# Kernel tuning notes

Hardware: AMD Instinct MI355X
Metric: run time of the kernel (lower is better)

## Reference

```python
import jax, jax.numpy as jnp
import numpy as np

HEADS = 16
DIM_HEAD = 64
DIM = 1024
EPS = 1e-5


def _layernorm(x, g, b):
    mu = jnp.mean(x, axis=-1, keepdims=True)
    var = jnp.var(x, axis=-1, keepdims=True)
    return (x - mu) * jax.lax.rsqrt(var + EPS) * g + b


def setup_inputs() -> dict:
    key = jax.random.key(0)
    ks = jax.random.split(key, 8)
    inner = HEADS * DIM_HEAD  # 1024
    x = jax.random.normal(ks[0], (2, 2048, DIM), dtype=jnp.float32)
    w_qkv = jax.random.normal(ks[1], (DIM, inner * 3), dtype=jnp.float32) * (DIM ** -0.5)
    w_out = jax.random.normal(ks[2], (inner, DIM), dtype=jnp.float32) * (inner ** -0.5)
    ln1_g = jnp.ones((DIM,), jnp.float32)
    ln1_b = jnp.zeros((DIM,), jnp.float32)
    ln2_g = jnp.ones((DIM,), jnp.float32)
    ln2_b = jnp.zeros((DIM,), jnp.float32)
    return {"x": x, "ln1_g": ln1_g, "ln1_b": ln1_b, "w_qkv": w_qkv,
            "w_out": w_out, "ln2_g": ln2_g, "ln2_b": ln2_b}


def reference(x, ln1_g, ln1_b, w_qkv, w_out, ln2_g, ln2_b):
    b, n, _ = x.shape
    scale = DIM_HEAD ** -0.5
    xn = _layernorm(x, ln1_g, ln1_b)
    qkv = xn @ w_qkv  # [b, n, 3*inner]
    q, k, v = jnp.split(qkv, 3, axis=-1)
    # b n (h d) -> b h n d
    resh = lambda t: t.reshape(b, n, HEADS, DIM_HEAD).transpose(0, 2, 1, 3)
    q, k, v = resh(q) * scale, resh(k), resh(v)
    sim = jnp.einsum('bhid,bhjd->bhij', q, k)
    causal = jnp.tril(jnp.ones((n, n), dtype=bool))
    # masked_fill(triu(1), 0) followed by relu == relu masked to lower triangle
    attn = jnp.where(causal, jax.nn.relu(sim), 0.0)
    out = jnp.einsum('bhij,bhjd->bhid', attn, v)
    out = out.transpose(0, 2, 1, 3).reshape(b, n, HEADS * DIM_HEAD)
    return _layernorm(out @ w_out, ln2_g, ln2_b)
```

## Files before the change

kernel.cpp:

```cpp
#include <hip/hip_runtime.h>
#include <cstdint>
#include <cstddef>


typedef __bf16 bf16_t;
typedef __bf16 bf16x8 __attribute__((ext_vector_type(8)));
typedef __bf16 bf16x4 __attribute__((ext_vector_type(4)));
typedef float  f32x4  __attribute__((ext_vector_type(4)));

#define DEV_INLINE __device__ __forceinline__

DEV_INLINE void async_copy16(void* lds, const void* g) {
  __builtin_amdgcn_global_load_lds(
      (__attribute__((address_space(1))) void*)(g),
      (__attribute__((address_space(3))) void*)(lds), 16, 0, 0);
}

__global__ __launch_bounds__(256) void prep_kernel(
    const float* __restrict__ x, const float* __restrict__ g1,
    const float* __restrict__ b1, bf16_t* __restrict__ xn,
    const float* __restrict__ w_qkv, bf16_t* __restrict__ wqkvT,
    const float* __restrict__ w_out, bf16_t* __restrict__ woutT) {
  const int bid = blockIdx.x;
  const int t = threadIdx.x;
  if (bid < 4096) {
    const int w = t >> 6, l = t & 63;
    const float* xr = x + (size_t)bid * 1024;
    float4 v = *(const float4*)(xr + t * 4);
    float s  = v.x + v.y + v.z + v.w;
    float s2 = v.x * v.x + v.y * v.y + v.z * v.z + v.w * v.w;
    #pragma unroll
    for (int off = 32; off >= 1; off >>= 1) {
      s  += __shfl_down(s, off);
      s2 += __shfl_down(s2, off);
    }
    __shared__ float red[8];
    if (l == 0) { red[w] = s; red[4 + w] = s2; }
    __syncthreads();
    s  = red[0] + red[1] + red[2] + red[3];
    s2 = red[4] + red[5] + red[6] + red[7];
    float mu  = s * (1.0f / 1024.0f);
    float var = s2 * (1.0f / 1024.0f) - mu * mu;
    float rs  = rsqrtf(var + 1e-5f);
    float4 gv = *(const float4*)(g1 + t * 4);
    float4 bv = *(const float4*)(b1 + t * 4);
    bf16x4 o;
    o[0] = (bf16_t)((v.x - mu) * rs * gv.x + bv.x);
    o[1] = (bf16_t)((v.y - mu) * rs * gv.y + bv.y);
    o[2] = (bf16_t)((v.z - mu) * rs * gv.z + bv.z);
    o[3] = (bf16_t)((v.w - mu) * rs * gv.w + bv.w);
    *(bf16x4*)(xn + (size_t)bid * 1024 + t * 4) = o;
  } else {
    const float* wsrc; bf16_t* wdst; int N, tile;
    if (bid < 4864) { wsrc = w_qkv; wdst = wqkvT; N = 3072; tile = bid - 4096; }
    else            { wsrc = w_out; wdst = woutT; N = 1024; tile = bid - 4864; }
    const int ntiles = N >> 6;
    const int n0 = (tile % ntiles) * 64, k0 = (tile / ntiles) * 64;
    __shared__ __align__(16) float tl[64][68];
    #pragma unroll
    for (int c = 0; c < 4; ++c) {
      int idx = c * 256 + t;
      int r = idx >> 4, c4 = (idx & 15) * 4;
      *(float4*)&tl[r][c4] = *(const float4*)(wsrc + (size_t)(k0 + r) * N + n0 + c4);
    }
    __syncthreads();
    #pragma unroll
    for (int c = 0; c < 2; ++c) {
      int idx = c * 256 + t;
      int nl = idx >> 3, kc = (idx & 7) * 8;
      bf16x8 o;
      #pragma unroll
      for (int ii = 0; ii < 8; ++ii) o[ii] = (bf16_t)tl[kc + ii][nl];
      *(bf16x8*)(wdst + (size_t)(n0 + nl) * 1024 + k0 + kc) = o;
    }
  }
}

__global__ __launch_bounds__(256) void ln2_kernel(
    const bf16_t* __restrict__ z0, const bf16_t* __restrict__ z1,
    const float* __restrict__ g, const float* __restrict__ bta,
    float* __restrict__ out) {
  const int row = blockIdx.x;
  const int t = threadIdx.x, w = t >> 6, l = t & 63;
  bf16x4 a0 = *(const bf16x4*)(z0 + (size_t)row * 1024 + t * 4);
  bf16x4 a1 = *(const bf16x4*)(z1 + (size_t)row * 1024 + t * 4);
  float4 v;
  v.x = (float)a0[0] + (float)a1[0];
  v.y = (float)a0[1] + (float)a1[1];
  v.z = (float)a0[2] + (float)a1[2];
  v.w = (float)a0[3] + (float)a1[3];
  float s  = v.x + v.y + v.z + v.w;
  float s2 = v.x * v.x + v.y * v.y + v.z * v.z + v.w * v.w;
  #pragma unroll
  for (int off = 32; off >= 1; off >>= 1) {
    s  += __shfl_down(s, off);
    s2 += __shfl_down(s2, off);
  }
  __shared__ float red[8];
  if (l == 0) { red[w] = s; red[4 + w] = s2; }
  __syncthreads();
  s  = red[0] + red[1] + red[2] + red[3];
  s2 = red[4] + red[5] + red[6] + red[7];
  float mu  = s * (1.0f / 1024.0f);
  float var = s2 * (1.0f / 1024.0f) - mu * mu;
  float rs  = rsqrtf(var + 1e-5f);
  float4 gv = *(const float4*)(g + t * 4);
  float4 bv = *(const float4*)(bta + t * 4);
  float4 o;
  o.x = (v.x - mu) * rs * gv.x + bv.x;
  o.y = (v.y - mu) * rs * gv.y + bv.y;
  o.z = (v.z - mu) * rs * gv.z + bv.z;
  o.w = (v.w - mu) * rs * gv.w + bv.w;
  *(float4*)(out + (size_t)row * 1024 + t * 4) = o;
}

template <int EPI, int KSPLIT>
__global__ __launch_bounds__(256, 3) void gemm128_kernel(
    const bf16_t* __restrict__ A, const bf16_t* __restrict__ Bt,
    void* __restrict__ C0, void* __restrict__ C1, void* __restrict__ C2) {
  __shared__ __align__(16) bf16_t As[128 * 64];
  __shared__ __align__(16) bf16_t Bs[128 * 64];
  const int t = threadIdx.x;
  const int w = t >> 6, l = t & 63, l15 = l & 15, quad = l >> 4;
  const int wy = w >> 1, wx = w & 1;
  const int m0 = blockIdx.y * 128, n0 = blockIdx.x * 128;
  const int kz = (KSPLIT > 1) ? blockIdx.z : 0;
  const int kt0 = kz * (16 / KSPLIT), kt1 = kt0 + (16 / KSPLIT);

  const int r_l = l >> 3;
  const int u_src = (l & 7) ^ r_l;
  const int rswz = l15 & 7;

  f32x4 acc[4][4];
  #pragma unroll
  for (int i = 0; i < 4; ++i)
    #pragma unroll
    for (int j = 0; j < 4; ++j) acc[i][j] = (f32x4)0.0f;

  for (int kt = kt0; kt < kt1; ++kt) {
    __syncthreads();
    #pragma unroll
    for (int c = 0; c < 4; ++c) {
      int idx = w * 4 + c;
      int row = idx * 8 + r_l;
      async_copy16(&As[idx * 512], A + (size_t)(m0 + row) * 1024 + kt * 64 + u_src * 8);
      async_copy16(&Bs[idx * 512], Bt + (size_t)(n0 + row) * 1024 + kt * 64 + u_src * 8);
    }
    __syncthreads();
    #pragma unroll
    for (int kk = 0; kk < 2; ++kk) {
      bf16x8 af[4], bfr[4];
      #pragma unroll
      for (int i = 0; i < 4; ++i)
        af[i] = *(const bf16x8*)&As[(wy * 64 + i * 16 + l15) * 64 + (((kk * 4 + quad) ^ rswz) * 8)];
      #pragma unroll
      for (int j = 0; j < 4; ++j)
        bfr[j] = *(const bf16x8*)&Bs[(wx * 64 + j * 16 + l15) * 64 + (((kk * 4 + quad) ^ rswz) * 8)];
      #pragma unroll
      for (int i = 0; i < 4; ++i)
        #pragma unroll
        for (int j = 0; j < 4; ++j)
          acc[i][j] = __builtin_amdgcn_mfma_f32_16x16x32_bf16(af[i], bfr[j], acc[i][j], 0, 0, 0);
    }
  }

  if (EPI == 0) {
    bf16_t* C = (bf16_t*)(kz == 0 ? C0 : C1);
    #pragma unroll
    for (int i = 0; i < 4; ++i)
      #pragma unroll
      for (int j = 0; j < 4; ++j)
        #pragma unroll
        for (int r = 0; r < 4; ++r) {
          int m = m0 + wy * 64 + i * 16 + quad * 4 + r;
          int n = n0 + wx * 64 + j * 16 + l15;
          C[(size_t)m * 1024 + n] = (bf16_t)acc[i][j][r];
        }
  } else {
    int nb = n0 + wx * 64;
    int which = nb >> 10;
    int head = (nb & 1023) >> 6;
    const int bq = m0 >> 11;
    const int mb = (m0 & 2047) + wy * 64;
    if (which == 2) {
      bf16_t* dst = (bf16_t*)C2 + ((size_t)(bq * 16 + head)) * 64 * 2048;
      #pragma unroll
      for (int i = 0; i < 4; ++i)
        #pragma unroll
        for (int j = 0; j < 4; ++j) {
          bf16x4 pk;
          #pragma unroll
          for (int r = 0; r < 4; ++r) pk[r] = (bf16_t)acc[i][j][r];
          int d = j * 16 + l15;
          int pos = mb + i * 16 + quad * 4;
          *(bf16x4*)(dst + (size_t)d * 2048 + pos) = pk;
        }
    } else {
      bf16_t* dst = which == 0 ? (bf16_t*)C0 : (bf16_t*)C1;
      float sc = which == 0 ? 0.125f : 1.0f;
      #pragma unroll
      for (int i = 0; i < 4; ++i)
        #pragma unroll
        for (int j = 0; j < 4; ++j)
          #pragma unroll
          for (int r = 0; r < 4; ++r) {
            int pos = mb + i * 16 + quad * 4 + r;
            int d = j * 16 + l15;
            dst[(((size_t)(bq * 16 + head)) * 2048 + pos) * 64 + d] =
                (bf16_t)(acc[i][j][r] * sc);
          }
    }
  }
}

__global__ __launch_bounds__(256, 2) void attn_kernel(
    const bf16_t* __restrict__ q, const bf16_t* __restrict__ k,
    const bf16_t* __restrict__ vT, bf16_t* __restrict__ out) {
  __shared__ __align__(16) bf16_t Ks[2][64 * 64];
  __shared__ __align__(16) bf16_t Vts[2][64 * 64];
  __shared__ __align__(16) bf16_t Ss[64 * 72];

  const int h = blockIdx.x, b = blockIdx.z;
  const int j = (b == 0) ? blockIdx.y : 15 - blockIdx.y;
  const int t = threadIdx.x;
  const int w = t >> 6, l = t & 63, l15 = l & 15, quad = l >> 4;
  const size_t bh = (size_t)(b * 16 + h);
  const int rA = 2 * j, rB = 2 * j + 1;
  const int nt = 2 * j + 2;

  const int r_l = l >> 3;
  const int u_g = (l & 7) ^ r_l;
  const int rswz = l15 & 7;

  auto stage_tile = [&](int buf, int kt) {
    #pragma unroll
    for (int c = 0; c < 2; ++c) {
      int idx = w * 2 + c;
      int row = idx * 8 + r_l;
      async_copy16(&Ks[buf][idx * 512],
                   k + (bh * 2048 + kt * 64 + row) * 64 + u_g * 8);
      async_copy16(&Vts[buf][idx * 512],
                   vT + (bh * 64 + row) * 2048 + kt * 64 + u_g * 8);
    }
  };

  auto load_lds = [&](const bf16_t* Kb, const bf16_t* Vb,
                      bf16x8 (&bk)[2][4], bf16x8 (&bv)[2][4]) {
    #pragma unroll
    for (int kk = 0; kk < 2; ++kk)
      #pragma unroll
      for (int tj = 0; tj < 4; ++tj) {
        int u = ((kk * 4 + quad) ^ rswz) * 8;
        bk[kk][tj] = *(const bf16x8*)&Kb[(tj * 16 + l15) * 64 + u];
        bv[kk][tj] = *(const bf16x8*)&Vb[(tj * 16 + l15) * 64 + u];
      }
  };

  bf16x8 qa[2][2];
  {
    #pragma unroll
    for (int kk = 0; kk < 2; ++kk) {
      qa[0][kk] = *(const bf16x8*)(q + (bh * 2048 + rA * 64 + w * 16 + l15) * 64 + kk * 32 + quad * 8);
      qa[1][kk] = *(const bf16x8*)(q + (bh * 2048 + rB * 64 + w * 16 + l15) * 64 + kk * 32 + quad * 8);
    }
  }

  f32x4 acc0[4], acc1[4];
  #pragma unroll
  for (int tj = 0; tj < 4; ++tj) { acc0[tj] = (f32x4)0.0f; acc1[tj] = (f32x4)0.0f; }

  auto sU = [&](f32x4 (&sacc)[4], bf16x8 (&qf)[2], bf16x8 (&bk)[2][4]) {
    #pragma unroll
    for (int tj = 0; tj < 4; ++tj) sacc[tj] = (f32x4)0.0f;
    #pragma unroll
    for (int kk = 0; kk < 2; ++kk)
      #pragma unroll
      for (int tj = 0; tj < 4; ++tj)
        sacc[tj] = __builtin_amdgcn_mfma_f32_16x16x32_bf16(bk[kk][tj], qf[kk], sacc[tj], 0, 0, 0);
  };
  auto wU = [&](f32x4 (&sacc)[4], bool dg) {
    #pragma unroll
    for (int tj = 0; tj < 4; ++tj) {
      bf16x4 pk;
      #pragma unroll
      for (int r = 0; r < 4; ++r) {
        float v = fmaxf(sacc[tj][r], 0.0f);
        if (dg && (tj * 16 + quad * 4 + r > w * 16 + l15)) v = 0.0f;
        pk[r] = (bf16_t)v;
      }
      *(bf16x4*)&Ss[(w * 16 + l15) * 72 + tj * 16 + quad * 4] = pk;
    }
  };
  auto pU = [&](f32x4 (&accr)[4], bf16x8 (&bv)[2][4]) {
    #pragma unroll
    for (int kk = 0; kk < 2; ++kk) {
      bf16x8 as_ = *(const bf16x8*)&Ss[(w * 16 + l15) * 72 + kk * 32 + quad * 8];
      #pragma unroll
      for (int tj = 0; tj < 4; ++tj)
        accr[tj] = __builtin_amdgcn_mfma_f32_16x16x32_bf16(bv[kk][tj], as_, accr[tj], 0, 0, 0);
    }
  };

  stage_tile(0, 0);
  for (int it = 0; it < nt; ++it) {
    __syncthreads();
    if (it + 1 < nt) stage_tile((it + 1) & 1, it + 1);
    const int buf = it & 1;
    bf16x8 bk[2][4], bv[2][4];
    load_lds(Ks[buf], Vts[buf], bk, bv);
    if (it < rB) {
      f32x4 s0[4], s1[4];
      sU(s0, qa[0], bk);
      sU(s1, qa[1], bk);
      wU(s0, it == rA); pU(acc0, bv);
      wU(s1, false);    pU(acc1, bv);
    } else {
      f32x4 s1[4];
      sU(s1, qa[1], bk);
      wU(s1, true); pU(acc1, bv);
    }
  }

  #pragma unroll
  for (int tj = 0; tj < 4; ++tj) {
    bf16x4 p0, p1;
    #pragma unroll
    for (int r = 0; r < 4; ++r) { p0[r] = (bf16_t)acc0[tj][r]; p1[r] = (bf16_t)acc1[tj][r]; }
    int posA = rA * 64 + w * 16 + l15;
    int posB = rB * 64 + w * 16 + l15;
    int col = h * 64 + tj * 16 + quad * 4;
    *(bf16x4*)(out + ((size_t)b * 2048 + posA) * 1024 + col) = p0;
    *(bf16x4*)(out + ((size_t)b * 2048 + posB) * 1024 + col) = p1;
  }
}

extern "C" void kernel_launch(void* const* d_in, const int* in_sizes, int n_in,
                              void* d_out, int out_size, void* d_ws, size_t ws_size,
                              hipStream_t stream) {
  (void)in_sizes; (void)n_in; (void)out_size; (void)ws_size;
  const float* x     = (const float*)d_in[0];
  const float* ln1_g = (const float*)d_in[1];
  const float* ln1_b = (const float*)d_in[2];
  const float* w_qkv = (const float*)d_in[3];
  const float* w_out = (const float*)d_in[4];
  const float* ln2_g = (const float*)d_in[5];
  const float* ln2_b = (const float*)d_in[6];
  float* out = (float*)d_out;

  char* ws = (char*)d_ws;
  bf16_t* xn     = (bf16_t*)(ws + 0);
  bf16_t* wqkvT  = (bf16_t*)(ws + 8388608);
  bf16_t* woutT  = (bf16_t*)(ws + 14680064);
  bf16_t* qb     = (bf16_t*)(ws + 16777216);
  bf16_t* kb     = (bf16_t*)(ws + 25165824);
  bf16_t* vTb    = (bf16_t*)(ws + 41943040);
  bf16_t* ao     = (bf16_t*)(ws + 50331648);
  bf16_t* zb0    = (bf16_t*)(ws + 58720256);
  bf16_t* zb1    = (bf16_t*)(ws + 67108864);

  prep_kernel<<<5120, 256, 0, stream>>>(x, ln1_g, ln1_b, xn, w_qkv, wqkvT, w_out, woutT);
  gemm128_kernel<1, 1><<<dim3(24, 32), 256, 0, stream>>>(xn, wqkvT, qb, kb, vTb);
  attn_kernel<<<dim3(16, 16, 2), 256, 0, stream>>>(qb, kb, vTb, ao);
  gemm128_kernel<0, 2><<<dim3(8, 32, 2), 256, 0, stream>>>(ao, woutT, zb0, zb1, nullptr);
  ln2_kernel<<<4096, 256, 0, stream>>>(zb0, zb1, ln2_g, ln2_b, out);
}
```

Before: 184.6 us.

## Pair short and long causal query rows in 512-thread attention blocks sharing K/V tiles

Each attention block now has 8 waves covering two query-row pairs, j and 15-j, which balances causal work per block. K/V tiles are staged two at a time and shared by both halves, so the long half reuses the tiles the short half also needs. The grid is halved and blocks get twice the threads and LDS. Possible costs are lower occupancy from the larger LDS footprint and idle waves in the short half once its rows are finished.

```diff
diff --git a/kernel.cpp b/kernel.cpp
--- a/kernel.cpp
+++ b/kernel.cpp
@@ -213,34 +213,43 @@
   }
 }
 
-__global__ __launch_bounds__(256, 2) void attn_kernel(
+__global__ __launch_bounds__(512, 2) void attn_kernel(
     const bf16_t* __restrict__ q, const bf16_t* __restrict__ k,
     const bf16_t* __restrict__ vT, bf16_t* __restrict__ out) {
-  __shared__ __align__(16) bf16_t Ks[2][64 * 64];
-  __shared__ __align__(16) bf16_t Vts[2][64 * 64];
-  __shared__ __align__(16) bf16_t Ss[64 * 72];
-
-  const int h = blockIdx.x, b = blockIdx.z;
-  const int j = (b == 0) ? blockIdx.y : 15 - blockIdx.y;
+  __shared__ __align__(16) bf16_t Ks[2][2][64 * 64];
+  __shared__ __align__(16) bf16_t Vts[2][2][64 * 64];
+  __shared__ __align__(16) bf16_t Ss[2][64 * 72];
+
+  const int h = blockIdx.x, j = blockIdx.y, b = blockIdx.z;
   const int t = threadIdx.x;
   const int w = t >> 6, l = t & 63, l15 = l & 15, quad = l >> 4;
+  const int pairSel = w >> 2;
+  const int wl = w & 3;
   const size_t bh = (size_t)(b * 16 + h);
-  const int rA = 2 * j, rB = 2 * j + 1;
-  const int nt = 2 * j + 2;
+  const int r0 = pairSel ? 30 - 2 * j : 2 * j;
+  const int r1 = r0 + 1;
+  const int niter = 16 - j;
 
   const int r_l = l >> 3;
   const int u_g = (l & 7) ^ r_l;
   const int rswz = l15 & 7;
 
-  auto stage_tile = [&](int buf, int kt) {
-    #pragma unroll
-    for (int c = 0; c < 2; ++c) {
-      int idx = w * 2 + c;
+  auto stage_pair = [&](int buf, int i2) {
+    #pragma unroll
+    for (int c = 0; c < 4; ++c) {
+      int op = w * 4 + c;
+      int tau = op >> 4;
+      int rem = op & 15;
+      int mK = rem >> 3;
+      int idx = rem & 7;
+      int kt = 2 * i2 + tau;
       int row = idx * 8 + r_l;
-      async_copy16(&Ks[buf][idx * 512],
-                   k + (bh * 2048 + kt * 64 + row) * 64 + u_g * 8);
-      async_copy16(&Vts[buf][idx * 512],
-                   vT + (bh * 64 + row) * 2048 + kt * 64 + u_g * 8);
+      if (mK == 0)
+        async_copy16(&Ks[buf][tau][idx * 512],
+                     k + (bh * 2048 + kt * 64 + row) * 64 + u_g * 8);
+      else
+        async_copy16(&Vts[buf][tau][idx * 512],
+                     vT + (bh * 64 + row) * 2048 + kt * 64 + u_g * 8);
     }
   };
 
@@ -260,8 +269,8 @@
   {
     #pragma unroll
     for (int kk = 0; kk < 2; ++kk) {
-      qa[0][kk] = *(const bf16x8*)(q + (bh * 2048 + rA * 64 + w * 16 + l15) * 64 + kk * 32 + quad * 8);
-      qa[1][kk] = *(const bf16x8*)(q + (bh * 2048 + rB * 64 + w * 16 + l15) * 64 + kk * 32 + quad * 8);
+      qa[0][kk] = *(const bf16x8*)(q + (bh * 2048 + r0 * 64 + wl * 16 + l15) * 64 + kk * 32 + quad * 8);
+      qa[1][kk] = *(const bf16x8*)(q + (bh * 2048 + r1 * 64 + wl * 16 + l15) * 64 + kk * 32 + quad * 8);
     }
   }
 
@@ -285,39 +294,44 @@
       #pragma unroll
       for (int r = 0; r < 4; ++r) {
         float v = fmaxf(sacc[tj][r], 0.0f);
-        if (dg && (tj * 16 + quad * 4 + r > w * 16 + l15)) v = 0.0f;
+        if (dg && (tj * 16 + quad * 4 + r > wl * 16 + l15)) v = 0.0f;
         pk[r] = (bf16_t)v;
       }
-      *(bf16x4*)&Ss[(w * 16 + l15) * 72 + tj * 16 + quad * 4] = pk;
+      *(bf16x4*)&Ss[pairSel][(wl * 16 + l15) * 72 + tj * 16 + quad * 4] = pk;
     }
   };
   auto pU = [&](f32x4 (&accr)[4], bf16x8 (&bv)[2][4]) {
     #pragma unroll
     for (int kk = 0; kk < 2; ++kk) {
-      bf16x8 as_ = *(const bf16x8*)&Ss[(w * 16 + l15) * 72 + kk * 32 + quad * 8];
+      bf16x8 as_ = *(const bf16x8*)&Ss[pairSel][(wl * 16 + l15) * 72 + kk * 32 + quad * 8];
       #pragma unroll
       for (int tj = 0; tj < 4; ++tj)
         accr[tj] = __builtin_amdgcn_mfma_f32_16x16x32_bf16(bv[kk][tj], as_, accr[tj], 0, 0, 0);
     }
   };
 
-  stage_tile(0, 0);
-  for (int it = 0; it < nt; ++it) {
-    __syncthreads();
-    if (it + 1 < nt) stage_tile((it + 1) & 1, it + 1);
-    const int buf = it & 1;
-    bf16x8 bk[2][4], bv[2][4];
-    load_lds(Ks[buf], Vts[buf], bk, bv);
-    if (it < rB) {
-      f32x4 s0[4], s1[4];
-      sU(s0, qa[0], bk);
-      sU(s1, qa[1], bk);
-      wU(s0, it == rA); pU(acc0, bv);
-      wU(s1, false);    pU(acc1, bv);
-    } else {
-      f32x4 s1[4];
-      sU(s1, qa[1], bk);
-      wU(s1, true); pU(acc1, bv);
+  stage_pair(0, 0);
+  for (int i = 0; i < niter; ++i) {
+    __syncthreads();
+    if (i + 1 < niter) stage_pair((i + 1) & 1, i + 1);
+    const int buf = i & 1;
+    #pragma unroll
+    for (int tau = 0; tau < 2; ++tau) {
+      const int kt = 2 * i + tau;
+      if (kt > r1) continue;
+      bf16x8 bk[2][4], bv[2][4];
+      load_lds(Ks[buf][tau], Vts[buf][tau], bk, bv);
+      if (kt < r1) {
+        f32x4 s0[4], s1[4];
+        sU(s0, qa[0], bk);
+        sU(s1, qa[1], bk);
+        wU(s0, kt == r0); pU(acc0, bv);
+        wU(s1, false);    pU(acc1, bv);
+      } else {
+        f32x4 s1[4];
+        sU(s1, qa[1], bk);
+        wU(s1, true); pU(acc1, bv);
+      }
     }
   }
 
@@ -326,8 +340,8 @@
     bf16x4 p0, p1;
     #pragma unroll
     for (int r = 0; r < 4; ++r) { p0[r] = (bf16_t)acc0[tj][r]; p1[r] = (bf16_t)acc1[tj][r]; }
-    int posA = rA * 64 + w * 16 + l15;
-    int posB = rB * 64 + w * 16 + l15;
+    int posA = r0 * 64 + wl * 16 + l15;
+    int posB = r1 * 64 + wl * 16 + l15;
     int col = h * 64 + tj * 16 + quad * 4;
     *(bf16x4*)(out + ((size_t)b * 2048 + posA) * 1024 + col) = p0;
     *(bf16x4*)(out + ((size_t)b * 2048 + posB) * 1024 + col) = p1;
@@ -360,7 +374,7 @@
 
   prep_kernel<<<5120, 256, 0, stream>>>(x, ln1_g, ln1_b, xn, w_qkv, wqkvT, w_out, woutT);
   gemm128_kernel<1, 1><<<dim3(24, 32), 256, 0, stream>>>(xn, wqkvT, qb, kb, vTb);
-  attn_kernel<<<dim3(16, 16, 2), 256, 0, stream>>>(qb, kb, vTb, ao);
+  attn_kernel<<<dim3(16, 8, 2), 512, 0, stream>>>(qb, kb, vTb, ao);
   gemm128_kernel<0, 2><<<dim3(8, 32, 2), 256, 0, stream>>>(ao, woutT, zb0, zb1, nullptr);
   ln2_kernel<<<4096, 256, 0, stream>>>(zb0, zb1, ln2_g, ln2_b, out);
 }
```

Result: faster. 171.4 us (-7.2%).

## Pair short and long causal query tiles per block to balance attention work

Applied to the files above, without the earlier changes.

Each attention block now handles query tiles m and 31-m instead of two adjacent tiles 2j and 2j+1. This evens out the causal-mask work across blocks, so the heaviest block no longer processes nearly twice the tiles of an average block. The score scratch buffer is split per wave and per query tile, so both score tiles are written before either PV product is computed. The K/V staging loop is reorganised so each wave issues only K or only V copies. The longest block still streams all 32 KV tiles, so the benefit depends on compute rather than load latency dominating.

```diff
diff --git a/kernel.cpp b/kernel.cpp
--- a/kernel.cpp
+++ b/kernel.cpp
@@ -218,15 +218,15 @@
     const bf16_t* __restrict__ vT, bf16_t* __restrict__ out) {
   __shared__ __align__(16) bf16_t Ks[2][64 * 64];
   __shared__ __align__(16) bf16_t Vts[2][64 * 64];
-  __shared__ __align__(16) bf16_t Ss[64 * 72];
-
-  const int h = blockIdx.x, b = blockIdx.z;
-  const int j = (b == 0) ? blockIdx.y : 15 - blockIdx.y;
+  __shared__ __align__(16) bf16_t Ss[4][2][16 * 72];
+
+  const int x = blockIdx.x, h = blockIdx.y, b = blockIdx.z;
+  const int m = ((x & 1) == 0) ? (x >> 1) : 15 - (x >> 1);
   const int t = threadIdx.x;
   const int w = t >> 6, l = t & 63, l15 = l & 15, quad = l >> 4;
   const size_t bh = (size_t)(b * 16 + h);
-  const int rA = 2 * j, rB = 2 * j + 1;
-  const int nt = 2 * j + 2;
+  const int r_lo = m, r_hi = 31 - m;
+  const int niter = 32 - m;
 
   const int r_l = l >> 3;
   const int u_g = (l & 7) ^ r_l;
@@ -234,13 +234,17 @@
 
   auto stage_tile = [&](int buf, int kt) {
     #pragma unroll
-    for (int c = 0; c < 2; ++c) {
-      int idx = w * 2 + c;
+    for (int c = 0; c < 4; ++c) {
+      int op = w * 4 + c;
+      int mK = op >> 3;
+      int idx = op & 7;
       int row = idx * 8 + r_l;
-      async_copy16(&Ks[buf][idx * 512],
-                   k + (bh * 2048 + kt * 64 + row) * 64 + u_g * 8);
-      async_copy16(&Vts[buf][idx * 512],
-                   vT + (bh * 64 + row) * 2048 + kt * 64 + u_g * 8);
+      if (mK == 0)
+        async_copy16(&Ks[buf][idx * 512],
+                     k + (bh * 2048 + kt * 64 + row) * 64 + u_g * 8);
+      else
+        async_copy16(&Vts[buf][idx * 512],
+                     vT + (bh * 64 + row) * 2048 + kt * 64 + u_g * 8);
     }
   };
 
@@ -260,8 +264,8 @@
   {
     #pragma unroll
     for (int kk = 0; kk < 2; ++kk) {
-      qa[0][kk] = *(const bf16x8*)(q + (bh * 2048 + rA * 64 + w * 16 + l15) * 64 + kk * 32 + quad * 8);
-      qa[1][kk] = *(const bf16x8*)(q + (bh * 2048 + rB * 64 + w * 16 + l15) * 64 + kk * 32 + quad * 8);
+      qa[0][kk] = *(const bf16x8*)(q + (bh * 2048 + r_lo * 64 + w * 16 + l15) * 64 + kk * 32 + quad * 8);
+      qa[1][kk] = *(const bf16x8*)(q + (bh * 2048 + r_hi * 64 + w * 16 + l15) * 64 + kk * 32 + quad * 8);
     }
   }
 
@@ -278,7 +282,7 @@
       for (int tj = 0; tj < 4; ++tj)
         sacc[tj] = __builtin_amdgcn_mfma_f32_16x16x32_bf16(bk[kk][tj], qf[kk], sacc[tj], 0, 0, 0);
   };
-  auto wU = [&](f32x4 (&sacc)[4], bool dg) {
+  auto wU = [&](f32x4 (&sacc)[4], bool dg, bf16_t* SsBuf) {
     #pragma unroll
     for (int tj = 0; tj < 4; ++tj) {
       bf16x4 pk;
@@ -288,36 +292,42 @@
         if (dg && (tj * 16 + quad * 4 + r > w * 16 + l15)) v = 0.0f;
         pk[r] = (bf16_t)v;
       }
-      *(bf16x4*)&Ss[(w * 16 + l15) * 72 + tj * 16 + quad * 4] = pk;
-    }
-  };
-  auto pU = [&](f32x4 (&accr)[4], bf16x8 (&bv)[2][4]) {
+      *(bf16x4*)&SsBuf[l15 * 72 + tj * 16 + quad * 4] = pk;
+    }
+  };
+  auto pU = [&](f32x4 (&accr)[4], bf16x8 (&bv)[2][4], const bf16_t* SsBuf) {
     #pragma unroll
     for (int kk = 0; kk < 2; ++kk) {
-      bf16x8 as_ = *(const bf16x8*)&Ss[(w * 16 + l15) * 72 + kk * 32 + quad * 8];
+      bf16x8 as_ = *(const bf16x8*)&SsBuf[l15 * 72 + kk * 32 + quad * 8];
       #pragma unroll
       for (int tj = 0; tj < 4; ++tj)
         accr[tj] = __builtin_amdgcn_mfma_f32_16x16x32_bf16(bv[kk][tj], as_, accr[tj], 0, 0, 0);
     }
   };
 
+  bf16_t* SsA = &Ss[w][0][0];
+  bf16_t* SsB = &Ss[w][1][0];
+
   stage_tile(0, 0);
-  for (int it = 0; it < nt; ++it) {
-    __syncthreads();
-    if (it + 1 < nt) stage_tile((it + 1) & 1, it + 1);
-    const int buf = it & 1;
+  for (int kt = 0; kt < niter; ++kt) {
+    __syncthreads();
+    if (kt + 1 < niter) stage_tile((kt + 1) & 1, kt + 1);
+    const int buf = kt & 1;
     bf16x8 bk[2][4], bv[2][4];
     load_lds(Ks[buf], Vts[buf], bk, bv);
-    if (it < rB) {
+    if (kt <= r_lo) {
       f32x4 s0[4], s1[4];
       sU(s0, qa[0], bk);
       sU(s1, qa[1], bk);
-      wU(s0, it == rA); pU(acc0, bv);
-      wU(s1, false);    pU(acc1, bv);
+      wU(s0, kt == r_lo, SsA);
+      wU(s1, kt == r_hi, SsB);
+      pU(acc0, bv, SsA);
+      pU(acc1, bv, SsB);
     } else {
       f32x4 s1[4];
       sU(s1, qa[1], bk);
-      wU(s1, true); pU(acc1, bv);
+      wU(s1, kt == r_hi, SsB);
+      pU(acc1, bv, SsB);
     }
   }
 
@@ -326,8 +336,8 @@
     bf16x4 p0, p1;
     #pragma unroll
     for (int r = 0; r < 4; ++r) { p0[r] = (bf16_t)acc0[tj][r]; p1[r] = (bf16_t)acc1[tj][r]; }
-    int posA = rA * 64 + w * 16 + l15;
-    int posB = rB * 64 + w * 16 + l15;
+    int posA = r_lo * 64 + w * 16 + l15;
+    int posB = r_hi * 64 + w * 16 + l15;
     int col = h * 64 + tj * 16 + quad * 4;
     *(bf16x4*)(out + ((size_t)b * 2048 + posA) * 1024 + col) = p0;
     *(bf16x4*)(out + ((size_t)b * 2048 + posB) * 1024 + col) = p1;
```

After: 187.9 us. No clear change (+1.8%).
